# Kernel optimization log

Measured on AMD Instinct MI355X. Metric: run time of the kernel, lower is better.

## Reference

```python
import jax, jax.numpy as jnp
import numpy as np

N = 100000   # nodes
E = 1600000  # edges (avg degree 16)
IN, H, C = 256, 64, 47


def setup_inputs() -> dict:
    key = jax.random.key(0)
    k0, k1, k2, k3 = jax.random.split(key, 4)
    x = jax.random.normal(k0, (N, IN), dtype=jnp.float32)
    edge_index = jax.random.randint(k1, (2, E), 0, N, dtype=jnp.int32)
    # GCNConv params (glorot-ish weights, zero bias as in PyG default)
    W1 = jax.random.normal(k2, (IN, H), dtype=jnp.float32) / np.sqrt(IN).astype(np.float32)
    b1 = jnp.zeros((H,), jnp.float32)
    W2 = jax.random.normal(k3, (H, C), dtype=jnp.float32) / np.sqrt(H).astype(np.float32)
    b2 = jnp.zeros((C,), jnp.float32)
    return {"x": x, "W1": W1, "b1": b1, "W2": W2, "b2": b2, "edge_index": edge_index}


def gcn_conv(x, W, b, src, dst):
    """GCNConv: transform, then symmetric-normalized aggregation with self-loops."""
    n = x.shape[0]
    h = x @ W  # [n, out]
    loop = jnp.arange(n, dtype=src.dtype)
    s = jnp.concatenate([src, loop])  # add self-loops
    d = jnp.concatenate([dst, loop])
    deg = jax.ops.segment_sum(jnp.ones_like(d, dtype=h.dtype), d, num_segments=n)
    dinv = jnp.where(deg > 0, jax.lax.rsqrt(deg), 0.0)
    norm = dinv[s] * dinv[d]  # [E+n]
    msg = h[s] * norm[:, None]  # gather + scale (irregular, memory-bound)
    out = jax.ops.segment_sum(msg, d, num_segments=n)
    return out + b


def reference(x, W1, b1, W2, b2, edge_index):
    src, dst = edge_index[0], edge_index[1]
    h = jax.nn.relu(gcn_conv(x, W1, b1, src, dst))
    # F.dropout(training=self.training): inference mode -> identity
    out = gcn_conv(h, W2, b2, src, dst)
    return jax.nn.log_softmax(out, axis=1)
```

## Files before the change

kernel.cpp:

```cpp
#include <hip/hip_runtime.h>
#include <math.h>

#define N_NODES 100000
#define N_EDGES 1600000
#define DIM_IN  256
#define DIM_H   64
#define DIM_C   47
#define DIM_CP  48
#define NB       8
#define BUCKET_W 12500
#define BCAP     204000
#define CHUNK_P1 1024
#define SEG_P2   2048
#define NSEG_P2  100
#define CHUNK_NODES 250
#define NCHUNK   400
#define CCAP     4608
#define XBP      264

typedef __attribute__((ext_vector_type(8))) short bf16x8;
typedef __attribute__((ext_vector_type(4))) float f32x4;

static __device__ __forceinline__ unsigned short f2bf(float f) {
  unsigned u = __builtin_bit_cast(unsigned, f);
  u += 0x7FFFu + ((u >> 16) & 1u);
  return (unsigned short)(u >> 16);
}
static __device__ __forceinline__ float bf2f(unsigned short h) {
  unsigned u = ((unsigned)h) << 16;
  return __builtin_bit_cast(float, u);
}

__global__ __launch_bounds__(512) void k_zero(int* __restrict__ bucket_cur,
                                              int* __restrict__ chunk_cur) {
  if (threadIdx.x < NB) bucket_cur[threadIdx.x] = 0;
  if (threadIdx.x < NCHUNK) chunk_cur[threadIdx.x] = 0;
}

__global__ __launch_bounds__(256) void k_bin(const int* __restrict__ src,
                                             const int* __restrict__ dst,
                                             int* __restrict__ bucket_cur,
                                             unsigned* __restrict__ bucket_buf) {
  __shared__ int lcnt[NB], lbase[NB], lcur[NB];
  if (threadIdx.x < NB) lcnt[threadIdx.x] = 0;
  __syncthreads();
  const int base = blockIdx.x * CHUNK_P1 + threadIdx.x;
  int dreg[4], sreg[4];
#pragma unroll
  for (int it = 0; it < 4; ++it) {
    int e = base + it * 256;
    int d = -1, s = 0;
    if (e < N_EDGES) { d = dst[e]; s = src[e]; }
    dreg[it] = d; sreg[it] = s;
    if (d >= 0) atomicAdd(&lcnt[d / BUCKET_W], 1);
  }
  __syncthreads();
  if (threadIdx.x < NB) {
    lbase[threadIdx.x] = atomicAdd(&bucket_cur[threadIdx.x], lcnt[threadIdx.x]);
    lcur[threadIdx.x] = 0;
  }
  __syncthreads();
#pragma unroll
  for (int it = 0; it < 4; ++it) {
    int d = dreg[it];
    if (d >= 0) {
      int b = d / BUCKET_W;
      int r = atomicAdd(&lcur[b], 1);
      unsigned pack = ((unsigned)(d - b * BUCKET_W) << 17) | (unsigned)sreg[it];
      bucket_buf[(size_t)b * BCAP + lbase[b] + r] = pack;
    }
  }
}

__global__ __launch_bounds__(256) void k_bin2(const unsigned* __restrict__ bucket_buf,
                                              const int* __restrict__ bucket_cnt,
                                              int* __restrict__ chunk_cur,
                                              unsigned* __restrict__ chunk_buf) {
  const int b   = blockIdx.x / NSEG_P2;
  const int seg = blockIdx.x % NSEG_P2;
  const int n_b = bucket_cnt[b];
  const int s0  = seg * SEG_P2;
  const int s1  = (n_b < s0 + SEG_P2) ? n_b : (s0 + SEG_P2);
  __shared__ int lcnt[50], lbase[50], lcur[50];
  if (threadIdx.x < 50) lcnt[threadIdx.x] = 0;
  __syncthreads();
  unsigned preg[8]; int creg[8];
#pragma unroll
  for (int it = 0; it < 8; ++it) {
    int i = s0 + it * 256 + (int)threadIdx.x;
    unsigned p = 0; int cl = -1;
    if (i < s1) { p = bucket_buf[(size_t)b * BCAP + i]; cl = (int)(p >> 17) / CHUNK_NODES; atomicAdd(&lcnt[cl], 1); }
    preg[it] = p; creg[it] = cl;
  }
  __syncthreads();
  if (threadIdx.x < 50) {
    lbase[threadIdx.x] = atomicAdd(&chunk_cur[b * 50 + threadIdx.x], lcnt[threadIdx.x]);
    lcur[threadIdx.x] = 0;
  }
  __syncthreads();
#pragma unroll
  for (int it = 0; it < 8; ++it) {
    int cl = creg[it];
    if (cl >= 0) {
      unsigned p = preg[it];
      int dl = (int)(p >> 17) - cl * CHUNK_NODES;
      int r = atomicAdd(&lcur[cl], 1);
      chunk_buf[(size_t)(b * 50 + cl) * CCAP + lbase[cl] + r] =
          ((unsigned)dl << 17) | (p & 0x1FFFFu);
    }
  }
}

__global__ __launch_bounds__(512) void k_scan_chunks(const int* __restrict__ chunk_cur,
                                                     int* __restrict__ chunk_base) {
  __shared__ int ls[512];
  const int tid = threadIdx.x;
  int v = (tid < NCHUNK) ? chunk_cur[tid] : 0;
  ls[tid] = v;
  __syncthreads();
  for (int off = 1; off < 512; off <<= 1) {
    int u = (tid >= off) ? ls[tid - off] : 0;
    __syncthreads();
    ls[tid] += u;
    __syncthreads();
  }
  if (tid < NCHUNK) chunk_base[tid] = ls[tid] - v;
}

__global__ __launch_bounds__(256) void k_sort_chunk(const unsigned* __restrict__ chunk_buf,
                                                    const int* __restrict__ chunk_cur,
                                                    const int* __restrict__ chunk_base,
                                                    int* __restrict__ cnt,
                                                    int* __restrict__ row_start,
                                                    int* __restrict__ sorted_src) {
  const int c    = blockIdx.x;
  const int n_c  = chunk_cur[c];
  const int base = chunk_base[c];
  const unsigned* buf = chunk_buf + (size_t)c * CCAP;
  __shared__ int cntA[256], exclA[256], curA[256];
  __shared__ int sortedL[CCAP];
  const int tid = threadIdx.x;
  cntA[tid] = 0; curA[tid] = 0;
  __syncthreads();
  for (int i = tid; i < n_c; i += 256) atomicAdd(&cntA[buf[i] >> 17], 1);
  __syncthreads();
  int myc = cntA[tid];
  exclA[tid] = myc;
  __syncthreads();
  for (int off = 1; off < 256; off <<= 1) {
    int u = (tid >= off) ? exclA[tid - off] : 0;
    __syncthreads();
    exclA[tid] += u;
    __syncthreads();
  }
  int excl = exclA[tid] - myc;
  if (tid < CHUNK_NODES) {
    int n = c * CHUNK_NODES + tid;
    cnt[n] = myc;
    row_start[n] = base + excl;
  }
  __syncthreads();
  exclA[tid] = excl;
  __syncthreads();
  for (int i = tid; i < n_c; i += 256) {
    unsigned p = buf[i];
    int dl = (int)(p >> 17);
    int pos = exclA[dl] + atomicAdd(&curA[dl], 1);
    sortedL[pos] = (int)(p & 0x1FFFFu);
  }
  __syncthreads();
  for (int i = tid; i < n_c; i += 256) sorted_src[base + i] = sortedL[i];
}

__global__ __launch_bounds__(256) void k_dinv(const int* __restrict__ cnt,
                                              float* __restrict__ dinv) {
  int i = blockIdx.x * 256 + threadIdx.x;
  if (i < N_NODES) dinv[i] = rsqrtf((float)cnt[i] + 1.0f);
}

__global__ __launch_bounds__(256) void k_padW2(const float* __restrict__ W2,
                                               float* __restrict__ W2p) {
  int i = blockIdx.x * 256 + threadIdx.x;
  if (i >= DIM_H * DIM_CP) return;
  int k = i / DIM_CP, j = i % DIM_CP;
  W2p[i] = (j < DIM_C) ? W2[k * DIM_C + j] : 0.f;
}

__global__ __launch_bounds__(256) void k_prepW1(const float* __restrict__ W1,
                                                short* __restrict__ W1f) {
  int i = blockIdx.x * 256 + threadIdx.x;
  if (i >= 4 * 8 * 64 * 8) return;
  int e    = i & 7;
  int lane = (i >> 3) & 63;
  int ks   = (i >> 9) & 7;
  int wv   = i >> 12;
  int col  = wv * 16 + (lane & 15);
  int k    = ks * 32 + (lane >> 4) * 8 + e;
  W1f[i] = (short)f2bf(W1[k * DIM_H + col]);
}

__global__ __launch_bounds__(256) void k_gemm1(const float* __restrict__ x,
                                               const short* __restrict__ W1f,
                                               const float* __restrict__ dinv,
                                               unsigned short* __restrict__ h1b) {
  __shared__ unsigned short xb[64][XBP];
  const int lane = threadIdx.x & 63;
  const int wv   = threadIdx.x >> 6;
  const int m16  = lane & 15;
  const int kb   = lane >> 4;
  const int base_row = blockIdx.x * 64;

#pragma unroll 4
  for (int i = 0; i < 16; ++i) {
    int r = i * 4 + wv;
    int grow = base_row + r;
    if (grow >= N_NODES) grow = N_NODES - 1;
    float4 v = *(const float4*)(x + (size_t)grow * DIM_IN + lane * 4);
    ushort4 b;
    b.x = f2bf(v.x); b.y = f2bf(v.y); b.z = f2bf(v.z); b.w = f2bf(v.w);
    *(ushort4*)&xb[r][lane * 4] = b;
  }
  __syncthreads();

  const bf16x8* wf = (const bf16x8*)W1f + (size_t)wv * 8 * 64 + lane;
  f32x4 c0 = {0.f, 0.f, 0.f, 0.f}, c1 = c0, c2 = c0, c3 = c0;
#pragma unroll
  for (int ks = 0; ks < 8; ++ks) {
    bf16x8 bb = wf[ks * 64];
#pragma unroll
    for (int rg = 0; rg < 4; ++rg) {
      bf16x8 af = *(const bf16x8*)&xb[rg * 16 + m16][ks * 32 + kb * 8];
      if (rg == 0) c0 = __builtin_amdgcn_mfma_f32_16x16x32_bf16(af, bb, c0, 0, 0, 0);
      if (rg == 1) c1 = __builtin_amdgcn_mfma_f32_16x16x32_bf16(af, bb, c1, 0, 0, 0);
      if (rg == 2) c2 = __builtin_amdgcn_mfma_f32_16x16x32_bf16(af, bb, c2, 0, 0, 0);
      if (rg == 3) c3 = __builtin_amdgcn_mfma_f32_16x16x32_bf16(af, bb, c3, 0, 0, 0);
    }
  }

  const int j0 = wv * 16 + m16;
#pragma unroll
  for (int rg = 0; rg < 4; ++rg) {
    f32x4 c = (rg == 0) ? c0 : (rg == 1) ? c1 : (rg == 2) ? c2 : c3;
#pragma unroll
    for (int r = 0; r < 4; ++r) {
      int row = base_row + rg * 16 + kb * 4 + r;
      if (row < N_NODES) h1b[(size_t)row * DIM_H + j0] = f2bf(c[r] * dinv[row]);
    }
  }
}

__global__ __launch_bounds__(256) void k_agg1_gather(const unsigned short* __restrict__ h1b,
                                                     const float* __restrict__ dinv,
                                                     const float* __restrict__ b1,
                                                     const int* __restrict__ row_start,
                                                     const int* __restrict__ cnt,
                                                     const int* __restrict__ sorted_src,
                                                     float* __restrict__ agg1) {
  int n = blockIdx.x * 4 + (threadIdx.x >> 6);
  int j = threadIdx.x & 63;
  if (n >= N_NODES) return;
  int start = row_start[n];
  int deg   = cnt[n];
  float acc0 = bf2f(h1b[(size_t)n * DIM_H + j]);
  float acc1 = 0.f, acc2 = 0.f, acc3 = 0.f;
  float acc4 = 0.f, acc5 = 0.f, acc6 = 0.f, acc7 = 0.f;
  int k = 0;
  for (; k + 8 <= deg; k += 8) {
    int s0 = sorted_src[start + k + 0];
    int s1 = sorted_src[start + k + 1];
    int s2 = sorted_src[start + k + 2];
    int s3 = sorted_src[start + k + 3];
    int s4 = sorted_src[start + k + 4];
    int s5 = sorted_src[start + k + 5];
    int s6 = sorted_src[start + k + 6];
    int s7 = sorted_src[start + k + 7];
    acc0 += bf2f(h1b[(size_t)s0 * DIM_H + j]);
    acc1 += bf2f(h1b[(size_t)s1 * DIM_H + j]);
    acc2 += bf2f(h1b[(size_t)s2 * DIM_H + j]);
    acc3 += bf2f(h1b[(size_t)s3 * DIM_H + j]);
    acc4 += bf2f(h1b[(size_t)s4 * DIM_H + j]);
    acc5 += bf2f(h1b[(size_t)s5 * DIM_H + j]);
    acc6 += bf2f(h1b[(size_t)s6 * DIM_H + j]);
    acc7 += bf2f(h1b[(size_t)s7 * DIM_H + j]);
  }
  for (; k + 2 <= deg; k += 2) {
    int s0 = sorted_src[start + k + 0];
    int s1 = sorted_src[start + k + 1];
    acc0 += bf2f(h1b[(size_t)s0 * DIM_H + j]);
    acc1 += bf2f(h1b[(size_t)s1 * DIM_H + j]);
  }
  for (; k < deg; ++k)
    acc0 += bf2f(h1b[(size_t)sorted_src[start + k] * DIM_H + j]);
  float di = dinv[n];
  agg1[(size_t)n * DIM_H + j] =
      di * (((acc0 + acc1) + (acc2 + acc3)) + ((acc4 + acc5) + (acc6 + acc7))) + b1[j];
}

__global__ __launch_bounds__(192) void k_gemm2(const float* __restrict__ agg1,
                                               const float* __restrict__ W2p,
                                               const float* __restrict__ dinv,
                                               unsigned short* __restrict__ h2b) {
  const int lane = threadIdx.x & 63;
  const int j0   = __builtin_amdgcn_readfirstlane((threadIdx.x >> 6) * 16);
  int row = blockIdx.x * 64 + lane;
  if (row >= N_NODES) row = N_NODES - 1;
  const float4* xr = (const float4*)(agg1 + (size_t)row * DIM_H);

  float4 xv[16];
#pragma unroll
  for (int k4 = 0; k4 < 16; ++k4) xv[k4] = xr[k4];
  __builtin_amdgcn_sched_barrier(0);

  float acc[16];
#pragma unroll
  for (int j = 0; j < 16; ++j) acc[j] = 0.f;

#pragma unroll
  for (int k4 = 0; k4 < DIM_H / 4; ++k4) {
    float4 v = xv[k4];
    v.x = fmaxf(v.x, 0.f); v.y = fmaxf(v.y, 0.f);
    v.z = fmaxf(v.z, 0.f); v.w = fmaxf(v.w, 0.f);
#pragma unroll
    for (int kk = 0; kk < 4; ++kk) {
      float xk = (kk == 0) ? v.x : (kk == 1) ? v.y : (kk == 2) ? v.z : v.w;
      const float* wrow = W2p + (size_t)(4 * k4 + kk) * DIM_CP + j0;
#pragma unroll
      for (int j = 0; j < 16; ++j)
        acc[j] = fmaf(xk, wrow[j], acc[j]);
    }
  }

  float di = dinv[row];
  unsigned* outp = (unsigned*)(h2b + (size_t)row * DIM_CP + j0);
#pragma unroll
  for (int p = 0; p < 8; ++p) {
    unsigned lo = f2bf(di * acc[2 * p]);
    unsigned hi = f2bf(di * acc[2 * p + 1]);
    outp[p] = lo | (hi << 16);
  }
}

__global__ __launch_bounds__(256) void k_agg2_gather(const unsigned short* __restrict__ h2b,
                                                     const float* __restrict__ dinv,
                                                     const float* __restrict__ b2,
                                                     const int* __restrict__ row_start,
                                                     const int* __restrict__ cnt,
                                                     const int* __restrict__ sorted_src,
                                                     float* __restrict__ out) {
  int n = blockIdx.x * 4 + (threadIdx.x >> 6);
  int j = threadIdx.x & 63;
  if (n >= N_NODES) return;
  int jj = (j < DIM_C) ? j : DIM_C;
  int start = row_start[n];
  int deg   = cnt[n];
  float acc0 = bf2f(h2b[(size_t)n * DIM_CP + jj]);
  float acc1 = 0.f, acc2 = 0.f, acc3 = 0.f;
  float acc4 = 0.f, acc5 = 0.f, acc6 = 0.f, acc7 = 0.f;
  int k = 0;
  for (; k + 8 <= deg; k += 8) {
    int s0 = sorted_src[start + k + 0];
    int s1 = sorted_src[start + k + 1];
    int s2 = sorted_src[start + k + 2];
    int s3 = sorted_src[start + k + 3];
    int s4 = sorted_src[start + k + 4];
    int s5 = sorted_src[start + k + 5];
    int s6 = sorted_src[start + k + 6];
    int s7 = sorted_src[start + k + 7];
    acc0 += bf2f(h2b[(size_t)s0 * DIM_CP + jj]);
    acc1 += bf2f(h2b[(size_t)s1 * DIM_CP + jj]);
    acc2 += bf2f(h2b[(size_t)s2 * DIM_CP + jj]);
    acc3 += bf2f(h2b[(size_t)s3 * DIM_CP + jj]);
    acc4 += bf2f(h2b[(size_t)s4 * DIM_CP + jj]);
    acc5 += bf2f(h2b[(size_t)s5 * DIM_CP + jj]);
    acc6 += bf2f(h2b[(size_t)s6 * DIM_CP + jj]);
    acc7 += bf2f(h2b[(size_t)s7 * DIM_CP + jj]);
  }
  for (; k + 2 <= deg; k += 2) {
    int s0 = sorted_src[start + k + 0];
    int s1 = sorted_src[start + k + 1];
    acc0 += bf2f(h2b[(size_t)s0 * DIM_CP + jj]);
    acc1 += bf2f(h2b[(size_t)s1 * DIM_CP + jj]);
  }
  for (; k < deg; ++k)
    acc0 += bf2f(h2b[(size_t)sorted_src[start + k] * DIM_CP + jj]);
  float di = dinv[n];
  float acc = di * (((acc0 + acc1) + (acc2 + acc3)) + ((acc4 + acc5) + (acc6 + acc7)))
            + ((j < DIM_C) ? b2[jj] : 0.f);

  float v = (j < DIM_C) ? acc : -INFINITY;
  float m = v;
  for (int o = 32; o; o >>= 1) m = fmaxf(m, __shfl_xor(m, o));
  float ex = (j < DIM_C) ? __expf(v - m) : 0.0f;
  float s = ex;
  for (int o = 32; o; o >>= 1) s += __shfl_xor(s, o);
  if (j < DIM_C) out[(size_t)n * DIM_C + j] = v - m - __logf(s);
}

extern "C" void kernel_launch(void* const* d_in, const int* in_sizes, int n_in,
                              void* d_out, int out_size, void* d_ws, size_t ws_size,
                              hipStream_t stream) {
  const float* x  = (const float*)d_in[0];
  const float* W1 = (const float*)d_in[1];
  const float* b1 = (const float*)d_in[2];
  const float* W2 = (const float*)d_in[3];
  const float* b2 = (const float*)d_in[4];
  const int*   ei = (const int*)d_in[5];
  const int* src = ei;
  const int* dst = ei + N_EDGES;
  float* out = (float*)d_out;

  float* ws   = (float*)d_ws;
  float* dinv = ws;
  float* W2p  = dinv + N_NODES;
  short* W1f  = (short*)(W2p + DIM_H * DIM_CP);
  unsigned short* h1b = (unsigned short*)(W1f + 16384);
  float* agg1 = (float*)(h1b + (size_t)N_NODES * DIM_H);
  unsigned short* h2b = h1b;
  unsigned* chunk_buf = (unsigned*)h1b;
  int* ibuf        = (int*)(agg1 + (size_t)N_NODES * DIM_H);
  int* cnt         = ibuf;
  int* row_start   = cnt + N_NODES;
  int* bucket_cur  = row_start + N_NODES;
  int* chunk_cur   = bucket_cur + 64;
  int* chunk_base  = chunk_cur + NCHUNK;
  int* sorted_src  = chunk_base + NCHUNK + 64;
  unsigned* bucket_buf = (unsigned*)(sorted_src + N_EDGES);

  const int nblk_n  = (N_NODES + 255) / 256;
  const int nblk_nw = (N_NODES + 3) / 4;
  const int nblk_g1 = (N_NODES + 63) / 64;
  const int nblk_g2 = (N_NODES + 63) / 64;
  const int nblk_p1 = (N_EDGES + CHUNK_P1 - 1) / CHUNK_P1;

  k_zero<<<1, 512, 0, stream>>>(bucket_cur, chunk_cur);
  k_bin<<<nblk_p1, 256, 0, stream>>>(src, dst, bucket_cur, bucket_buf);
  k_bin2<<<NB * NSEG_P2, 256, 0, stream>>>(bucket_buf, bucket_cur, chunk_cur, chunk_buf);
  k_scan_chunks<<<1, 512, 0, stream>>>(chunk_cur, chunk_base);
  k_sort_chunk<<<NCHUNK, 256, 0, stream>>>(chunk_buf, chunk_cur, chunk_base,
                                           cnt, row_start, sorted_src);
  k_dinv<<<nblk_n, 256, 0, stream>>>(cnt, dinv);
  k_padW2<<<(DIM_H * DIM_CP + 255) / 256, 256, 0, stream>>>(W2, W2p);
  k_prepW1<<<64, 256, 0, stream>>>(W1, W1f);

  k_gemm1<<<nblk_g1, 256, 0, stream>>>(x, W1f, dinv, h1b);
  k_agg1_gather<<<nblk_nw, 256, 0, stream>>>(h1b, dinv, b1, row_start, cnt, sorted_src, agg1);

  k_gemm2<<<nblk_g2, 192, 0, stream>>>(agg1, W2p, dinv, h2b);
  k_agg2_gather<<<nblk_nw, 256, 0, stream>>>(h2b, dinv, b2, row_start, cnt, sorted_src, out);
}
```

Measured before the change: 236.3 us.

## Gather layer-1 neighbours with 16-byte row loads and LDS slot reduction

Rewrites the layer-1 aggregation so each wave covers 8 neighbour slots at once, with each lane loading 8 bf16 features (one uint4) instead of one 2-byte element per lane. Per-slot partial sums are reduced through shared memory. Out-of-range slots point at a zero row appended after h1b, which a new tiny kernel clears, so the loop needs no branches. The aim is fewer, wider memory transactions and more loads in flight per wave, at the cost of a __syncthreads, LDS traffic, one extra launch and a shifted workspace layout.

```diff
diff --git a/kernel.cpp b/kernel.cpp
--- a/kernel.cpp
+++ b/kernel.cpp
@@ -30,6 +30,12 @@
   unsigned u = ((unsigned)h) << 16;
   return __builtin_bit_cast(float, u);
 }
+static __device__ __forceinline__ float blo(unsigned u) {
+  return __builtin_bit_cast(float, u << 16);
+}
+static __device__ __forceinline__ float bhi(unsigned u) {
+  return __builtin_bit_cast(float, u & 0xffff0000u);
+}
 
 __global__ __launch_bounds__(512) void k_zero(int* __restrict__ bucket_cur,
                                               int* __restrict__ chunk_cur) {
@@ -178,6 +184,10 @@
   if (i < N_NODES) dinv[i] = rsqrtf((float)cnt[i] + 1.0f);
 }
 
+__global__ __launch_bounds__(64) void k_zrow(unsigned short* __restrict__ h1b) {
+  h1b[(size_t)N_NODES * DIM_H + threadIdx.x] = 0;
+}
+
 __global__ __launch_bounds__(256) void k_padW2(const float* __restrict__ W2,
                                                float* __restrict__ W2p) {
   int i = blockIdx.x * 256 + threadIdx.x;
@@ -256,44 +266,37 @@
                                                      const int* __restrict__ cnt,
                                                      const int* __restrict__ sorted_src,
                                                      float* __restrict__ agg1) {
-  int n = blockIdx.x * 4 + (threadIdx.x >> 6);
-  int j = threadIdx.x & 63;
-  if (n >= N_NODES) return;
-  int start = row_start[n];
-  int deg   = cnt[n];
-  float acc0 = bf2f(h1b[(size_t)n * DIM_H + j]);
-  float acc1 = 0.f, acc2 = 0.f, acc3 = 0.f;
-  float acc4 = 0.f, acc5 = 0.f, acc6 = 0.f, acc7 = 0.f;
-  int k = 0;
-  for (; k + 8 <= deg; k += 8) {
-    int s0 = sorted_src[start + k + 0];
-    int s1 = sorted_src[start + k + 1];
-    int s2 = sorted_src[start + k + 2];
-    int s3 = sorted_src[start + k + 3];
-    int s4 = sorted_src[start + k + 4];
-    int s5 = sorted_src[start + k + 5];
-    int s6 = sorted_src[start + k + 6];
-    int s7 = sorted_src[start + k + 7];
-    acc0 += bf2f(h1b[(size_t)s0 * DIM_H + j]);
-    acc1 += bf2f(h1b[(size_t)s1 * DIM_H + j]);
-    acc2 += bf2f(h1b[(size_t)s2 * DIM_H + j]);
-    acc3 += bf2f(h1b[(size_t)s3 * DIM_H + j]);
-    acc4 += bf2f(h1b[(size_t)s4 * DIM_H + j]);
-    acc5 += bf2f(h1b[(size_t)s5 * DIM_H + j]);
-    acc6 += bf2f(h1b[(size_t)s6 * DIM_H + j]);
-    acc7 += bf2f(h1b[(size_t)s7 * DIM_H + j]);
-  }
-  for (; k + 2 <= deg; k += 2) {
-    int s0 = sorted_src[start + k + 0];
-    int s1 = sorted_src[start + k + 1];
-    acc0 += bf2f(h1b[(size_t)s0 * DIM_H + j]);
-    acc1 += bf2f(h1b[(size_t)s1 * DIM_H + j]);
-  }
-  for (; k < deg; ++k)
-    acc0 += bf2f(h1b[(size_t)sorted_src[start + k] * DIM_H + j]);
-  float di = dinv[n];
-  agg1[(size_t)n * DIM_H + j] =
-      di * (((acc0 + acc1) + (acc2 + acc3)) + ((acc4 + acc5) + (acc6 + acc7))) + b1[j];
+  __shared__ float red[4][8][72];
+  const int wv   = threadIdx.x >> 6;
+  const int n    = blockIdx.x * 4 + wv;
+  const int lane = threadIdx.x & 63;
+  const int slot = lane >> 3, grp = lane & 7;
+  const int start = row_start[n];
+  const int deg   = cnt[n];
+  const int rounds = (deg + 8) >> 3;
+
+  float p0 = 0.f, p1 = 0.f, p2 = 0.f, p3 = 0.f, p4 = 0.f, p5 = 0.f, p6 = 0.f, p7 = 0.f;
+  int row0 = (slot == 0) ? n : ((slot <= deg) ? sorted_src[start + slot - 1] : N_NODES);
+  uint4 q = *((const uint4*)(h1b + (size_t)row0 * DIM_H) + grp);
+  for (int r = 1; r < rounds; ++r) {
+    int k = r * 8 + slot;
+    int row = (k <= deg) ? sorted_src[start + k - 1] : N_NODES;
+    uint4 qn = *((const uint4*)(h1b + (size_t)row * DIM_H) + grp);
+    p0 += blo(q.x); p1 += bhi(q.x); p2 += blo(q.y); p3 += bhi(q.y);
+    p4 += blo(q.z); p5 += bhi(q.z); p6 += blo(q.w); p7 += bhi(q.w);
+    q = qn;
+  }
+  p0 += blo(q.x); p1 += bhi(q.x); p2 += blo(q.y); p3 += bhi(q.y);
+  p4 += blo(q.z); p5 += bhi(q.z); p6 += blo(q.w); p7 += bhi(q.w);
+
+  float* rs = &red[wv][slot][grp * 8];
+  rs[0] = p0; rs[1] = p1; rs[2] = p2; rs[3] = p3;
+  rs[4] = p4; rs[5] = p5; rs[6] = p6; rs[7] = p7;
+  __syncthreads();
+  float v = 0.f;
+#pragma unroll
+  for (int s = 0; s < 8; ++s) v += red[wv][s][lane];
+  agg1[(size_t)n * DIM_H + lane] = dinv[n] * v + b1[lane];
 }
 
 __global__ __launch_bounds__(192) void k_gemm2(const float* __restrict__ agg1,
@@ -414,7 +417,7 @@
   float* W2p  = dinv + N_NODES;
   short* W1f  = (short*)(W2p + DIM_H * DIM_CP);
   unsigned short* h1b = (unsigned short*)(W1f + 16384);
-  float* agg1 = (float*)(h1b + (size_t)N_NODES * DIM_H);
+  float* agg1 = (float*)(h1b + (size_t)(N_NODES + 1) * DIM_H);
   unsigned short* h2b = h1b;
   unsigned* chunk_buf = (unsigned*)h1b;
   int* ibuf        = (int*)(agg1 + (size_t)N_NODES * DIM_H);
@@ -441,6 +444,7 @@
   k_dinv<<<nblk_n, 256, 0, stream>>>(cnt, dinv);
   k_padW2<<<(DIM_H * DIM_CP + 255) / 256, 256, 0, stream>>>(W2, W2p);
   k_prepW1<<<64, 256, 0, stream>>>(W1, W1f);
+  k_zrow<<<1, 64, 0, stream>>>(h1b);
 
   k_gemm1<<<nblk_g1, 256, 0, stream>>>(x, W1f, dinv, h1b);
   k_agg1_gather<<<nblk_nw, 256, 0, stream>>>(h1b, dinv, b1, row_start, cnt, sorted_src, agg1);
```

Result: faster. 223.2 us (-5.5%).
